# Kernel optimization log

Hardware: AMD Instinct MI355X
Metric: run time of the kernel (lower is better)

Reference implementation:

```python
import jax, jax.numpy as jnp
import numpy as np

N, D, K = 65536, 64, 1024
BB, HH, WW = 64, 32, 32


def setup_inputs() -> dict:
    key = jax.random.key(0)
    k1, k2 = jax.random.split(key)
    x = jax.random.normal(k1, (N, D), dtype=jnp.float32)
    # embedding initialized uniform(-1/K, 1/K)
    weight = jax.random.uniform(k2, (K, D), dtype=jnp.float32, minval=-1.0 / K, maxval=1.0 / K)
    return {"x": x, "weight": weight, "B": BB, "H": HH, "W": WW}


def reference(x, weight, B, H, W):
    beta = 1.0
    # pairwise squared distances [N, K]
    distances = (jnp.sum(x ** 2, axis=1, keepdims=True)
                 + jnp.sum(weight ** 2, axis=1)
                 - 2.0 * x @ weight.T)
    encoding_indices = jnp.argmin(distances, axis=1)  # [N]
    # one-hot @ weight is just a gather
    quantized = weight[encoding_indices]  # [N, D]
    e_latent_loss = jnp.mean((jax.lax.stop_gradient(quantized) - x) ** 2)
    q_latent_loss = jnp.mean((jax.lax.stop_gradient(x) - quantized) ** 2)
    loss = q_latent_loss + beta * e_latent_loss
    # straight-through estimator
    quantized = x + jax.lax.stop_gradient(quantized - x)
    quantized = quantized.reshape(B, H, W, D).transpose(0, 3, 1, 2)  # [B, D, H, W]
    return loss, quantized, encoding_indices[:, None]
```

## Files before the change

kernel.cpp:

```cpp
#include <hip/hip_runtime.h>

#define N_ROWS 65536
#define DIM 64
#define KCB 1024
#define Q_ELEMS 4194304
#define RPB 128
#define KQ 256
#define TILE 32
#define NTILES 8


__device__ __forceinline__ float np_pairwise_sumsq64(const float* v) {
#pragma clang fp contract(off)
    float r[8];
#pragma unroll
    for (int j = 0; j < 8; ++j) r[j] = v[j] * v[j];
#pragma unroll
    for (int i = 8; i < 64; i += 8) {
#pragma unroll
        for (int j = 0; j < 8; ++j) {
            float s = v[i + j] * v[i + j];
            r[j] = r[j] + s;
        }
    }
    return ((r[0] + r[1]) + (r[2] + r[3])) + ((r[4] + r[5]) + (r[6] + r[7]));
}

__global__ __launch_bounds__(64) void wnorm_kernel(const float* __restrict__ w,
                                                   float* __restrict__ wn2) {
    __shared__ float tile[64][65];
    const int t = threadIdx.x;
    const size_t base = (size_t)blockIdx.x * 64 * DIM;
#pragma unroll 4
    for (int i = 0; i < 64; ++i)
        tile[i][t] = w[base + (size_t)i * DIM + t];
    __syncthreads();
    float v[DIM];
#pragma unroll
    for (int d = 0; d < DIM; ++d) v[d] = tile[t][d];
    wn2[blockIdx.x * 64 + t] = np_pairwise_sumsq64(v);
}

__global__ __launch_bounds__(256, 2) void vq_kernel(const float* __restrict__ x,
                                                    const float* __restrict__ w,
                                                    const float* __restrict__ wn2,
                                                    float* __restrict__ out,
                                                    float* __restrict__ partial) {
    __shared__ float wtile[4][TILE * DIM];

    const int t = threadIdx.x;
    const int lane = t & 63;
    const int wv = t >> 6;
    const int rowbase = blockIdx.x * RPB;
    const int r0 = rowbase + lane;
    const int r1 = r0 + 64;

    float xr0[DIM], xr1[DIM];
    const float4* xv0 = (const float4*)(x + (size_t)r0 * DIM);
    const float4* xv1 = (const float4*)(x + (size_t)r1 * DIM);
#pragma unroll
    for (int i = 0; i < 16; ++i) {
        float4 a = xv0[i];
        xr0[4 * i + 0] = a.x; xr0[4 * i + 1] = a.y; xr0[4 * i + 2] = a.z; xr0[4 * i + 3] = a.w;
        float4 b = xv1[i];
        xr1[4 * i + 0] = b.x; xr1[4 * i + 1] = b.y; xr1[4 * i + 2] = b.z; xr1[4 * i + 3] = b.w;
    }
    const float S0 = np_pairwise_sumsq64(xr0);
    const float S1 = np_pairwise_sumsq64(xr1);

    const int kbase = wv * KQ;
    float best0 = 3.4e38f, best1 = 3.4e38f;
    int bi0 = kbase, bi1 = kbase;

    for (int tile = 0; tile < NTILES; ++tile) {
        const float* gsrc = w + (size_t)(kbase + tile * TILE) * DIM;
        float* ldst = &wtile[wv][0];
#pragma unroll
        for (int j = 0; j < 8; ++j) {
            float4 v = *(const float4*)(gsrc + j * 256 + lane * 4);
            *(float4*)(ldst + j * 256 + lane * 4) = v;
        }

        for (int c = 0; c < TILE; c += 4) {
            const float* w0 = ldst + c * DIM;
            float a00 = 0.f, a01 = 0.f, a02 = 0.f, a03 = 0.f;
            float a10 = 0.f, a11 = 0.f, a12 = 0.f, a13 = 0.f;
#pragma unroll
            for (int d = 0; d < DIM; d += 4) {
                float4 u0 = *(const float4*)(w0 + 0 * DIM + d);
                float4 u1 = *(const float4*)(w0 + 1 * DIM + d);
                float4 u2 = *(const float4*)(w0 + 2 * DIM + d);
                float4 u3 = *(const float4*)(w0 + 3 * DIM + d);
                float p0 = xr0[d], p1 = xr0[d + 1], p2 = xr0[d + 2], p3 = xr0[d + 3];
                float q0 = xr1[d], q1 = xr1[d + 1], q2 = xr1[d + 2], q3 = xr1[d + 3];
                a00 = __builtin_fmaf(p0, u0.x, a00); a00 = __builtin_fmaf(p1, u0.y, a00);
                a00 = __builtin_fmaf(p2, u0.z, a00); a00 = __builtin_fmaf(p3, u0.w, a00);
                a01 = __builtin_fmaf(p0, u1.x, a01); a01 = __builtin_fmaf(p1, u1.y, a01);
                a01 = __builtin_fmaf(p2, u1.z, a01); a01 = __builtin_fmaf(p3, u1.w, a01);
                a02 = __builtin_fmaf(p0, u2.x, a02); a02 = __builtin_fmaf(p1, u2.y, a02);
                a02 = __builtin_fmaf(p2, u2.z, a02); a02 = __builtin_fmaf(p3, u2.w, a02);
                a03 = __builtin_fmaf(p0, u3.x, a03); a03 = __builtin_fmaf(p1, u3.y, a03);
                a03 = __builtin_fmaf(p2, u3.z, a03); a03 = __builtin_fmaf(p3, u3.w, a03);
                a10 = __builtin_fmaf(q0, u0.x, a10); a10 = __builtin_fmaf(q1, u0.y, a10);
                a10 = __builtin_fmaf(q2, u0.z, a10); a10 = __builtin_fmaf(q3, u0.w, a10);
                a11 = __builtin_fmaf(q0, u1.x, a11); a11 = __builtin_fmaf(q1, u1.y, a11);
                a11 = __builtin_fmaf(q2, u1.z, a11); a11 = __builtin_fmaf(q3, u1.w, a11);
                a12 = __builtin_fmaf(q0, u2.x, a12); a12 = __builtin_fmaf(q1, u2.y, a12);
                a12 = __builtin_fmaf(q2, u2.z, a12); a12 = __builtin_fmaf(q3, u2.w, a12);
                a13 = __builtin_fmaf(q0, u3.x, a13); a13 = __builtin_fmaf(q1, u3.y, a13);
                a13 = __builtin_fmaf(q2, u3.z, a13); a13 = __builtin_fmaf(q3, u3.w, a13);
            }
            const int k = kbase + tile * TILE + c;
            float wnA = wn2[k + 0], wnB = wn2[k + 1], wnC = wn2[k + 2], wnD = wn2[k + 3];
            float d00 = (S0 + wnA) - 2.0f * a00;
            float d01 = (S0 + wnB) - 2.0f * a01;
            float d02 = (S0 + wnC) - 2.0f * a02;
            float d03 = (S0 + wnD) - 2.0f * a03;
            if (d00 < best0) { best0 = d00; bi0 = k + 0; }
            if (d01 < best0) { best0 = d01; bi0 = k + 1; }
            if (d02 < best0) { best0 = d02; bi0 = k + 2; }
            if (d03 < best0) { best0 = d03; bi0 = k + 3; }
            float d10 = (S1 + wnA) - 2.0f * a10;
            float d11 = (S1 + wnB) - 2.0f * a11;
            float d12 = (S1 + wnC) - 2.0f * a12;
            float d13 = (S1 + wnD) - 2.0f * a13;
            if (d10 < best1) { best1 = d10; bi1 = k + 0; }
            if (d11 < best1) { best1 = d11; bi1 = k + 1; }
            if (d12 < best1) { best1 = d12; bi1 = k + 2; }
            if (d13 < best1) { best1 = d13; bi1 = k + 3; }
        }
    }

    __syncthreads();
    float* cbd = (float*)&wtile[0][0];
    int*   cbk = (int*)((char*)&wtile[0][0] + 2048);
    float* red = (float*)((char*)&wtile[0][0] + 4096);
    cbd[wv * 128 + lane]      = best0;  cbk[wv * 128 + lane]      = bi0;
    cbd[wv * 128 + 64 + lane] = best1;  cbk[wv * 128 + 64 + lane] = bi1;
    __syncthreads();

    float lsum = 0.f;
    if (t < 128) {
        const int rb = t;
        float bd = cbd[0 * 128 + rb]; int bk = cbk[0 * 128 + rb];
#pragma unroll
        for (int q = 1; q < 4; ++q) {
            float dq = cbd[q * 128 + rb]; int kq = cbk[q * 128 + rb];
            if (dq < bd) { bd = dq; bk = kq; }
        }
        float xcur[DIM];
        if (wv == 0) {
#pragma unroll
            for (int d = 0; d < DIM; ++d) xcur[d] = xr0[d];
        } else {
#pragma unroll
            for (int d = 0; d < DIM; ++d) xcur[d] = xr1[d];
        }
        const int n = rowbase + rb;
        const int b = n >> 10;
        const int hw = n & 1023;
        float* outq = out + 1 + (size_t)b * 65536 + hw;
        const float4* wr4 = (const float4*)(w + (size_t)bk * DIM);
#pragma unroll
        for (int i = 0; i < 16; ++i) {
            float4 u = wr4[i];
            float d0 = u.x - xcur[4 * i + 0];
            float d1 = u.y - xcur[4 * i + 1];
            float d2 = u.z - xcur[4 * i + 2];
            float d3 = u.w - xcur[4 * i + 3];
            lsum += d0 * d0; lsum += d1 * d1; lsum += d2 * d2; lsum += d3 * d3;
            outq[(size_t)(4 * i + 0) * 1024] = xcur[4 * i + 0] + d0;
            outq[(size_t)(4 * i + 1) * 1024] = xcur[4 * i + 1] + d1;
            outq[(size_t)(4 * i + 2) * 1024] = xcur[4 * i + 2] + d2;
            outq[(size_t)(4 * i + 3) * 1024] = xcur[4 * i + 3] + d3;
        }
        out[1 + Q_ELEMS + n] = (float)bk;
    }
#pragma unroll
    for (int off = 32; off > 0; off >>= 1) lsum += __shfl_down(lsum, off, 64);
    if (lane == 0) red[wv] = lsum;
    __syncthreads();
    if (t == 0) partial[blockIdx.x] = (red[0] + red[1]) + (red[2] + red[3]);
}

__global__ void finish_kernel(const float* __restrict__ partial, float* __restrict__ out) {
    float v = partial[threadIdx.x] + partial[threadIdx.x + 256];
#pragma unroll
    for (int off = 32; off > 0; off >>= 1) v += __shfl_down(v, off, 64);
    __shared__ float red[4];
    const int lane = threadIdx.x & 63;
    const int wv = threadIdx.x >> 6;
    if (lane == 0) red[wv] = v;
    __syncthreads();
    if (threadIdx.x == 0) {
        float total = (red[0] + red[1]) + (red[2] + red[3]);
        out[0] = total * (2.0f / (float)(N_ROWS * DIM));
    }
}

extern "C" void kernel_launch(void* const* d_in, const int* in_sizes, int n_in,
                              void* d_out, int out_size, void* d_ws, size_t ws_size,
                              hipStream_t stream) {
    const float* x = (const float*)d_in[0];
    const float* w = (const float*)d_in[1];
    float* out = (float*)d_out;

    char* ws = (char*)d_ws;
    float* wn2 = (float*)(ws + 0);
    float* partial = (float*)(ws + 4096);

    wnorm_kernel<<<KCB / 64, 64, 0, stream>>>(w, wn2);
    vq_kernel<<<N_ROWS / RPB, 256, 0, stream>>>(x, w, wn2, out, partial);
    finish_kernel<<<1, 256, 0, stream>>>(partial, out);
}
```

Before: 207.4 us.

## Read codebook via uniform global loads instead of LDS tiles, one row per lane

The VQ kernel stops staging codebook tiles in shared memory. Each lane now reads codebook rows straight from global memory at wave-uniform addresses, which the compiler can turn into scalar loads, and handles one x row instead of two. Blocks cover 64 rows, so the grid doubles, and the finish kernel is adjusted to sum 1024 partials. This removes LDS traffic and the per-tile copies, but halves register-level reuse of each codebook element across rows and doubles global and L2 reads of the codebook.

```diff
diff --git a/kernel.cpp b/kernel.cpp
--- a/kernel.cpp
+++ b/kernel.cpp
@@ -4,10 +4,9 @@
 #define DIM 64
 #define KCB 1024
 #define Q_ELEMS 4194304
-#define RPB 128
+#define RPB 64
+#define NWAVES 4
 #define KQ 256
-#define TILE 32
-#define NTILES 8
 
 
 __device__ __forceinline__ float np_pairwise_sumsq64(const float* v) {
@@ -41,158 +40,116 @@
     wn2[blockIdx.x * 64 + t] = np_pairwise_sumsq64(v);
 }
 
-__global__ __launch_bounds__(256, 2) void vq_kernel(const float* __restrict__ x,
-                                                    const float* __restrict__ w,
-                                                    const float* __restrict__ wn2,
-                                                    float* __restrict__ out,
-                                                    float* __restrict__ partial) {
-    __shared__ float wtile[4][TILE * DIM];
+__global__ __launch_bounds__(256, 2)
+void vq_kernel(const float* __restrict__ x,
+               const float* __restrict__ w,
+               const float* __restrict__ wn2,
+               float* __restrict__ out,
+               float* __restrict__ partial) {
+    __shared__ float cbd[NWAVES][64];
+    __shared__ int   cbk[NWAVES][64];
 
     const int t = threadIdx.x;
     const int lane = t & 63;
     const int wv = t >> 6;
     const int rowbase = blockIdx.x * RPB;
-    const int r0 = rowbase + lane;
-    const int r1 = r0 + 64;
+    const int r = rowbase + lane;
 
-    float xr0[DIM], xr1[DIM];
-    const float4* xv0 = (const float4*)(x + (size_t)r0 * DIM);
-    const float4* xv1 = (const float4*)(x + (size_t)r1 * DIM);
+    float xr[DIM];
+    const float4* xv = (const float4*)(x + (size_t)r * DIM);
 #pragma unroll
     for (int i = 0; i < 16; ++i) {
-        float4 a = xv0[i];
-        xr0[4 * i + 0] = a.x; xr0[4 * i + 1] = a.y; xr0[4 * i + 2] = a.z; xr0[4 * i + 3] = a.w;
-        float4 b = xv1[i];
-        xr1[4 * i + 0] = b.x; xr1[4 * i + 1] = b.y; xr1[4 * i + 2] = b.z; xr1[4 * i + 3] = b.w;
+        float4 a = xv[i];
+        xr[4 * i + 0] = a.x; xr[4 * i + 1] = a.y; xr[4 * i + 2] = a.z; xr[4 * i + 3] = a.w;
     }
-    const float S0 = np_pairwise_sumsq64(xr0);
-    const float S1 = np_pairwise_sumsq64(xr1);
+    const float S = np_pairwise_sumsq64(xr);
 
     const int kbase = wv * KQ;
-    float best0 = 3.4e38f, best1 = 3.4e38f;
-    int bi0 = kbase, bi1 = kbase;
+    float best = 3.4e38f;
+    int bi = kbase;
 
-    for (int tile = 0; tile < NTILES; ++tile) {
-        const float* gsrc = w + (size_t)(kbase + tile * TILE) * DIM;
-        float* ldst = &wtile[wv][0];
+    for (int q = 0; q < KQ / 4; ++q) {
+        const int k = kbase + q * 4;
+        const float* __restrict__ wk = w + (size_t)k * DIM;
+        float a0 = 0.f, a1 = 0.f, a2 = 0.f, a3 = 0.f;
 #pragma unroll
-        for (int j = 0; j < 8; ++j) {
-            float4 v = *(const float4*)(gsrc + j * 256 + lane * 4);
-            *(float4*)(ldst + j * 256 + lane * 4) = v;
+        for (int ph = 0; ph < 4; ++ph) {
+            float u0[16], u1[16], u2[16], u3[16];
+#pragma unroll
+            for (int j = 0; j < 16; ++j) {
+                u0[j] = wk[0 * DIM + ph * 16 + j];
+                u1[j] = wk[1 * DIM + ph * 16 + j];
+                u2[j] = wk[2 * DIM + ph * 16 + j];
+                u3[j] = wk[3 * DIM + ph * 16 + j];
+            }
+#pragma unroll
+            for (int j = 0; j < 16; ++j) {
+                const float xd = xr[ph * 16 + j];
+                a0 = __builtin_fmaf(xd, u0[j], a0);
+                a1 = __builtin_fmaf(xd, u1[j], a1);
+                a2 = __builtin_fmaf(xd, u2[j], a2);
+                a3 = __builtin_fmaf(xd, u3[j], a3);
+            }
         }
-
-        for (int c = 0; c < TILE; c += 4) {
-            const float* w0 = ldst + c * DIM;
-            float a00 = 0.f, a01 = 0.f, a02 = 0.f, a03 = 0.f;
-            float a10 = 0.f, a11 = 0.f, a12 = 0.f, a13 = 0.f;
-#pragma unroll
-            for (int d = 0; d < DIM; d += 4) {
-                float4 u0 = *(const float4*)(w0 + 0 * DIM + d);
-                float4 u1 = *(const float4*)(w0 + 1 * DIM + d);
-                float4 u2 = *(const float4*)(w0 + 2 * DIM + d);
-                float4 u3 = *(const float4*)(w0 + 3 * DIM + d);
-                float p0 = xr0[d], p1 = xr0[d + 1], p2 = xr0[d + 2], p3 = xr0[d + 3];
-                float q0 = xr1[d], q1 = xr1[d + 1], q2 = xr1[d + 2], q3 = xr1[d + 3];
-                a00 = __builtin_fmaf(p0, u0.x, a00); a00 = __builtin_fmaf(p1, u0.y, a00);
-                a00 = __builtin_fmaf(p2, u0.z, a00); a00 = __builtin_fmaf(p3, u0.w, a00);
-                a01 = __builtin_fmaf(p0, u1.x, a01); a01 = __builtin_fmaf(p1, u1.y, a01);
-                a01 = __builtin_fmaf(p2, u1.z, a01); a01 = __builtin_fmaf(p3, u1.w, a01);
-                a02 = __builtin_fmaf(p0, u2.x, a02); a02 = __builtin_fmaf(p1, u2.y, a02);
-                a02 = __builtin_fmaf(p2, u2.z, a02); a02 = __builtin_fmaf(p3, u2.w, a02);
-                a03 = __builtin_fmaf(p0, u3.x, a03); a03 = __builtin_fmaf(p1, u3.y, a03);
-                a03 = __builtin_fmaf(p2, u3.z, a03); a03 = __builtin_fmaf(p3, u3.w, a03);
-                a10 = __builtin_fmaf(q0, u0.x, a10); a10 = __builtin_fmaf(q1, u0.y, a10);
-                a10 = __builtin_fmaf(q2, u0.z, a10); a10 = __builtin_fmaf(q3, u0.w, a10);
-                a11 = __builtin_fmaf(q0, u1.x, a11); a11 = __builtin_fmaf(q1, u1.y, a11);
-                a11 = __builtin_fmaf(q2, u1.z, a11); a11 = __builtin_fmaf(q3, u1.w, a11);
-                a12 = __builtin_fmaf(q0, u2.x, a12); a12 = __builtin_fmaf(q1, u2.y, a12);
-                a12 = __builtin_fmaf(q2, u2.z, a12); a12 = __builtin_fmaf(q3, u2.w, a12);
-                a13 = __builtin_fmaf(q0, u3.x, a13); a13 = __builtin_fmaf(q1, u3.y, a13);
-                a13 = __builtin_fmaf(q2, u3.z, a13); a13 = __builtin_fmaf(q3, u3.w, a13);
-            }
-            const int k = kbase + tile * TILE + c;
-            float wnA = wn2[k + 0], wnB = wn2[k + 1], wnC = wn2[k + 2], wnD = wn2[k + 3];
-            float d00 = (S0 + wnA) - 2.0f * a00;
-            float d01 = (S0 + wnB) - 2.0f * a01;
-            float d02 = (S0 + wnC) - 2.0f * a02;
-            float d03 = (S0 + wnD) - 2.0f * a03;
-            if (d00 < best0) { best0 = d00; bi0 = k + 0; }
-            if (d01 < best0) { best0 = d01; bi0 = k + 1; }
-            if (d02 < best0) { best0 = d02; bi0 = k + 2; }
-            if (d03 < best0) { best0 = d03; bi0 = k + 3; }
-            float d10 = (S1 + wnA) - 2.0f * a10;
-            float d11 = (S1 + wnB) - 2.0f * a11;
-            float d12 = (S1 + wnC) - 2.0f * a12;
-            float d13 = (S1 + wnD) - 2.0f * a13;
-            if (d10 < best1) { best1 = d10; bi1 = k + 0; }
-            if (d11 < best1) { best1 = d11; bi1 = k + 1; }
-            if (d12 < best1) { best1 = d12; bi1 = k + 2; }
-            if (d13 < best1) { best1 = d13; bi1 = k + 3; }
-        }
+        float wnA = wn2[k + 0], wnB = wn2[k + 1], wnC = wn2[k + 2], wnD = wn2[k + 3];
+        float d0 = (S + wnA) - 2.0f * a0;
+        float d1 = (S + wnB) - 2.0f * a1;
+        float d2 = (S + wnC) - 2.0f * a2;
+        float d3 = (S + wnD) - 2.0f * a3;
+        if (d0 < best) { best = d0; bi = k + 0; }
+        if (d1 < best) { best = d1; bi = k + 1; }
+        if (d2 < best) { best = d2; bi = k + 2; }
+        if (d3 < best) { best = d3; bi = k + 3; }
     }
 
-    __syncthreads();
-    float* cbd = (float*)&wtile[0][0];
-    int*   cbk = (int*)((char*)&wtile[0][0] + 2048);
-    float* red = (float*)((char*)&wtile[0][0] + 4096);
-    cbd[wv * 128 + lane]      = best0;  cbk[wv * 128 + lane]      = bi0;
-    cbd[wv * 128 + 64 + lane] = best1;  cbk[wv * 128 + 64 + lane] = bi1;
+    cbd[wv][lane] = best;  cbk[wv][lane] = bi;
     __syncthreads();
 
-    float lsum = 0.f;
-    if (t < 128) {
-        const int rb = t;
-        float bd = cbd[0 * 128 + rb]; int bk = cbk[0 * 128 + rb];
+    if (wv == 0) {
+        float bd = cbd[0][lane]; int bk = cbk[0][lane];
 #pragma unroll
-        for (int q = 1; q < 4; ++q) {
-            float dq = cbd[q * 128 + rb]; int kq = cbk[q * 128 + rb];
+        for (int qq = 1; qq < NWAVES; ++qq) {
+            float dq = cbd[qq][lane]; int kq = cbk[qq][lane];
             if (dq < bd) { bd = dq; bk = kq; }
         }
-        float xcur[DIM];
-        if (wv == 0) {
-#pragma unroll
-            for (int d = 0; d < DIM; ++d) xcur[d] = xr0[d];
-        } else {
-#pragma unroll
-            for (int d = 0; d < DIM; ++d) xcur[d] = xr1[d];
-        }
-        const int n = rowbase + rb;
+        const int n = r;
         const int b = n >> 10;
         const int hw = n & 1023;
         float* outq = out + 1 + (size_t)b * 65536 + hw;
         const float4* wr4 = (const float4*)(w + (size_t)bk * DIM);
+        float lsum = 0.f;
 #pragma unroll
         for (int i = 0; i < 16; ++i) {
             float4 u = wr4[i];
-            float d0 = u.x - xcur[4 * i + 0];
-            float d1 = u.y - xcur[4 * i + 1];
-            float d2 = u.z - xcur[4 * i + 2];
-            float d3 = u.w - xcur[4 * i + 3];
+            float d0 = u.x - xr[4 * i + 0];
+            float d1 = u.y - xr[4 * i + 1];
+            float d2 = u.z - xr[4 * i + 2];
+            float d3 = u.w - xr[4 * i + 3];
             lsum += d0 * d0; lsum += d1 * d1; lsum += d2 * d2; lsum += d3 * d3;
-            outq[(size_t)(4 * i + 0) * 1024] = xcur[4 * i + 0] + d0;
-            outq[(size_t)(4 * i + 1) * 1024] = xcur[4 * i + 1] + d1;
-            outq[(size_t)(4 * i + 2) * 1024] = xcur[4 * i + 2] + d2;
-            outq[(size_t)(4 * i + 3) * 1024] = xcur[4 * i + 3] + d3;
+            outq[(size_t)(4 * i + 0) * 1024] = xr[4 * i + 0] + d0;
+            outq[(size_t)(4 * i + 1) * 1024] = xr[4 * i + 1] + d1;
+            outq[(size_t)(4 * i + 2) * 1024] = xr[4 * i + 2] + d2;
+            outq[(size_t)(4 * i + 3) * 1024] = xr[4 * i + 3] + d3;
         }
         out[1 + Q_ELEMS + n] = (float)bk;
+#pragma unroll
+        for (int off = 32; off > 0; off >>= 1) lsum += __shfl_down(lsum, off, 64);
+        if (lane == 0) partial[blockIdx.x] = lsum;
     }
-#pragma unroll
-    for (int off = 32; off > 0; off >>= 1) lsum += __shfl_down(lsum, off, 64);
-    if (lane == 0) red[wv] = lsum;
-    __syncthreads();
-    if (t == 0) partial[blockIdx.x] = (red[0] + red[1]) + (red[2] + red[3]);
 }
 
 __global__ void finish_kernel(const float* __restrict__ partial, float* __restrict__ out) {
-    float v = partial[threadIdx.x] + partial[threadIdx.x + 256];
+    const int t = threadIdx.x;
+    float v = (partial[2 * t] + partial[2 * t + 1])
+            + (partial[2 * (t + 256)] + partial[2 * (t + 256) + 1]);
 #pragma unroll
     for (int off = 32; off > 0; off >>= 1) v += __shfl_down(v, off, 64);
     __shared__ float red[4];
-    const int lane = threadIdx.x & 63;
-    const int wv = threadIdx.x >> 6;
+    const int lane = t & 63;
+    const int wv = t >> 6;
     if (lane == 0) red[wv] = v;
     __syncthreads();
-    if (threadIdx.x == 0) {
+    if (t == 0) {
         float total = (red[0] + red[1]) + (red[2] + red[3]);
         out[0] = total * (2.0f / (float)(N_ROWS * DIM));
     }
```

Measured after the change: 546.0 us. 2.63x slower.

## Rotate codebook rows across lanes with DPP instead of staging through LDS

Applied to the files above, without the earlier changes.

Each lane now holds one codebook row in registers and passes the rows around the wavefront with DPP row rotations and xor shuffles, so every lane meets all 64 codewords of a group without touching shared memory. The LDS weight tile and its load/store traffic go away, and the launch bounds change to one block per SIMD to make room for the extra registers. Because each lane sees the codewords in a different order, the argmin tie-break now compares indices explicitly. The cost is 64 DPP moves per codeword step and fewer resident waves.

```diff
diff --git a/kernel.cpp b/kernel.cpp
--- a/kernel.cpp
+++ b/kernel.cpp
@@ -5,9 +5,8 @@
 #define KCB 1024
 #define Q_ELEMS 4194304
 #define RPB 128
+#define NWAVES 4
 #define KQ 256
-#define TILE 32
-#define NTILES 8
 
 
 __device__ __forceinline__ float np_pairwise_sumsq64(const float* v) {
@@ -41,12 +40,22 @@
     wn2[blockIdx.x * 64 + t] = np_pairwise_sumsq64(v);
 }
 
-__global__ __launch_bounds__(256, 2) void vq_kernel(const float* __restrict__ x,
-                                                    const float* __restrict__ w,
-                                                    const float* __restrict__ wn2,
-                                                    float* __restrict__ out,
-                                                    float* __restrict__ partial) {
-    __shared__ float wtile[4][TILE * DIM];
+__device__ __forceinline__ float rot16f(float v) {
+    return __int_as_float(__builtin_amdgcn_mov_dpp(__float_as_int(v), 0x121, 0xf, 0xf, false));
+}
+__device__ __forceinline__ int rot16i(int v) {
+    return __builtin_amdgcn_mov_dpp(v, 0x121, 0xf, 0xf, false);
+}
+
+__global__ __launch_bounds__(256, 1)
+void vq_kernel(const float* __restrict__ x,
+               const float* __restrict__ w,
+               const float* __restrict__ wn2,
+               float* __restrict__ out,
+               float* __restrict__ partial) {
+    __shared__ float cbd[NWAVES][128];
+    __shared__ int   cbk[NWAVES][128];
+    __shared__ float red[NWAVES];
 
     const int t = threadIdx.x;
     const int lane = t & 63;
@@ -72,80 +81,62 @@
     float best0 = 3.4e38f, best1 = 3.4e38f;
     int bi0 = kbase, bi1 = kbase;
 
-    for (int tile = 0; tile < NTILES; ++tile) {
-        const float* gsrc = w + (size_t)(kbase + tile * TILE) * DIM;
-        float* ldst = &wtile[wv][0];
-#pragma unroll
-        for (int j = 0; j < 8; ++j) {
-            float4 v = *(const float4*)(gsrc + j * 256 + lane * 4);
-            *(float4*)(ldst + j * 256 + lane * 4) = v;
-        }
-
-        for (int c = 0; c < TILE; c += 4) {
-            const float* w0 = ldst + c * DIM;
-            float a00 = 0.f, a01 = 0.f, a02 = 0.f, a03 = 0.f;
-            float a10 = 0.f, a11 = 0.f, a12 = 0.f, a13 = 0.f;
-#pragma unroll
-            for (int d = 0; d < DIM; d += 4) {
-                float4 u0 = *(const float4*)(w0 + 0 * DIM + d);
-                float4 u1 = *(const float4*)(w0 + 1 * DIM + d);
-                float4 u2 = *(const float4*)(w0 + 2 * DIM + d);
-                float4 u3 = *(const float4*)(w0 + 3 * DIM + d);
-                float p0 = xr0[d], p1 = xr0[d + 1], p2 = xr0[d + 2], p3 = xr0[d + 3];
-                float q0 = xr1[d], q1 = xr1[d + 1], q2 = xr1[d + 2], q3 = xr1[d + 3];
-                a00 = __builtin_fmaf(p0, u0.x, a00); a00 = __builtin_fmaf(p1, u0.y, a00);
-                a00 = __builtin_fmaf(p2, u0.z, a00); a00 = __builtin_fmaf(p3, u0.w, a00);
-                a01 = __builtin_fmaf(p0, u1.x, a01); a01 = __builtin_fmaf(p1, u1.y, a01);
-                a01 = __builtin_fmaf(p2, u1.z, a01); a01 = __builtin_fmaf(p3, u1.w, a01);
-                a02 = __builtin_fmaf(p0, u2.x, a02); a02 = __builtin_fmaf(p1, u2.y, a02);
-                a02 = __builtin_fmaf(p2, u2.z, a02); a02 = __builtin_fmaf(p3, u2.w, a02);
-                a03 = __builtin_fmaf(p0, u3.x, a03); a03 = __builtin_fmaf(p1, u3.y, a03);
-                a03 = __builtin_fmaf(p2, u3.z, a03); a03 = __builtin_fmaf(p3, u3.w, a03);
-                a10 = __builtin_fmaf(q0, u0.x, a10); a10 = __builtin_fmaf(q1, u0.y, a10);
-                a10 = __builtin_fmaf(q2, u0.z, a10); a10 = __builtin_fmaf(q3, u0.w, a10);
-                a11 = __builtin_fmaf(q0, u1.x, a11); a11 = __builtin_fmaf(q1, u1.y, a11);
-                a11 = __builtin_fmaf(q2, u1.z, a11); a11 = __builtin_fmaf(q3, u1.w, a11);
-                a12 = __builtin_fmaf(q0, u2.x, a12); a12 = __builtin_fmaf(q1, u2.y, a12);
-                a12 = __builtin_fmaf(q2, u2.z, a12); a12 = __builtin_fmaf(q3, u2.w, a12);
-                a13 = __builtin_fmaf(q0, u3.x, a13); a13 = __builtin_fmaf(q1, u3.y, a13);
-                a13 = __builtin_fmaf(q2, u3.z, a13); a13 = __builtin_fmaf(q3, u3.w, a13);
+#pragma unroll 1
+    for (int g = 0; g < 4; ++g) {
+        const int gbase = kbase + g * 64;
+        float cw[DIM];
+        const float4* wrow = (const float4*)(w + (size_t)(gbase + lane) * DIM);
+#pragma unroll
+        for (int i = 0; i < 16; ++i) {
+            float4 u = wrow[i];
+            cw[4 * i + 0] = u.x; cw[4 * i + 1] = u.y; cw[4 * i + 2] = u.z; cw[4 * i + 3] = u.w;
+        }
+        float wk = wn2[gbase + lane];
+        int kid = gbase + lane;
+
+#pragma unroll
+        for (int sub = 0; sub < 4; ++sub) {
+#pragma unroll 1
+            for (int s = 0; s < 16; ++s) {
+                float a0 = xr0[0] * cw[0];
+                float a1 = xr1[0] * cw[0];
+#pragma unroll
+                for (int d = 1; d < DIM; ++d) {
+                    a0 = __builtin_fmaf(xr0[d], cw[d], a0);
+                    a1 = __builtin_fmaf(xr1[d], cw[d], a1);
+                }
+                float dd0 = (S0 + wk) - 2.0f * a0;
+                float dd1 = (S1 + wk) - 2.0f * a1;
+                bool u0 = (dd0 < best0) || (dd0 == best0 && kid < bi0);
+                if (u0) { best0 = dd0; bi0 = kid; }
+                bool u1 = (dd1 < best1) || (dd1 == best1 && kid < bi1);
+                if (u1) { best1 = dd1; bi1 = kid; }
+#pragma unroll
+                for (int d = 0; d < DIM; ++d) cw[d] = rot16f(cw[d]);
+                wk = rot16f(wk);
+                kid = rot16i(kid);
             }
-            const int k = kbase + tile * TILE + c;
-            float wnA = wn2[k + 0], wnB = wn2[k + 1], wnC = wn2[k + 2], wnD = wn2[k + 3];
-            float d00 = (S0 + wnA) - 2.0f * a00;
-            float d01 = (S0 + wnB) - 2.0f * a01;
-            float d02 = (S0 + wnC) - 2.0f * a02;
-            float d03 = (S0 + wnD) - 2.0f * a03;
-            if (d00 < best0) { best0 = d00; bi0 = k + 0; }
-            if (d01 < best0) { best0 = d01; bi0 = k + 1; }
-            if (d02 < best0) { best0 = d02; bi0 = k + 2; }
-            if (d03 < best0) { best0 = d03; bi0 = k + 3; }
-            float d10 = (S1 + wnA) - 2.0f * a10;
-            float d11 = (S1 + wnB) - 2.0f * a11;
-            float d12 = (S1 + wnC) - 2.0f * a12;
-            float d13 = (S1 + wnD) - 2.0f * a13;
-            if (d10 < best1) { best1 = d10; bi1 = k + 0; }
-            if (d11 < best1) { best1 = d11; bi1 = k + 1; }
-            if (d12 < best1) { best1 = d12; bi1 = k + 2; }
-            if (d13 < best1) { best1 = d13; bi1 = k + 3; }
-        }
-    }
-
-    __syncthreads();
-    float* cbd = (float*)&wtile[0][0];
-    int*   cbk = (int*)((char*)&wtile[0][0] + 2048);
-    float* red = (float*)((char*)&wtile[0][0] + 4096);
-    cbd[wv * 128 + lane]      = best0;  cbk[wv * 128 + lane]      = bi0;
-    cbd[wv * 128 + 64 + lane] = best1;  cbk[wv * 128 + 64 + lane] = bi1;
+            if (sub < 3) {
+                const int m = (sub == 1) ? 32 : 16;
+#pragma unroll
+                for (int d = 0; d < DIM; ++d) cw[d] = __shfl_xor(cw[d], m, 64);
+                wk = __shfl_xor(wk, m, 64);
+                kid = __shfl_xor(kid, m, 64);
+            }
+        }
+    }
+
+    cbd[wv][lane]      = best0;  cbk[wv][lane]      = bi0;
+    cbd[wv][64 + lane] = best1;  cbk[wv][64 + lane] = bi1;
     __syncthreads();
 
     float lsum = 0.f;
     if (t < 128) {
         const int rb = t;
-        float bd = cbd[0 * 128 + rb]; int bk = cbk[0 * 128 + rb];
-#pragma unroll
-        for (int q = 1; q < 4; ++q) {
-            float dq = cbd[q * 128 + rb]; int kq = cbk[q * 128 + rb];
+        float bd = cbd[0][rb]; int bk = cbk[0][rb];
+#pragma unroll
+        for (int q = 1; q < NWAVES; ++q) {
+            float dq = cbd[q][rb]; int kq = cbk[q][rb];
             if (dq < bd) { bd = dq; bk = kq; }
         }
         float xcur[DIM];
```

After: 273.3 us. 1.32x slower.
